# Kernel optimization log

Hardware: AMD Instinct MI355X
Metric: run time of the kernel (lower is better)

Reference implementation:

```python
import jax, jax.numpy as jnp
import numpy as np

NUM_HEADS = 8
EMBED_DIM = 512
EXPAND = 3
RPE_DIM = 512
RPE_LAYERS = 3
B, N = 4, 2048
D1 = (EXPAND * EMBED_DIM) // NUM_HEADS * NUM_HEADS  # 1536
HEAD_DIM = D1 // NUM_HEADS  # 192


def srms(x):
    # SimpleRMSNorm: x / (||x||_2 * d^{-1/2} + eps)
    d = x.shape[-1]
    rms = jnp.linalg.norm(x, axis=-1, keepdims=True) * (d ** -0.5)
    return x / (rms + 1e-8)


def rpe_net(idx, Wp, bp, Wl, bl, Wr, br):
    # idx: (m, 1) relative positions -> (m, h*head_dim)
    h = idx @ Wp.T + bp
    for i in range(Wl.shape[0]):  # fixed small layer count
        h = jax.nn.relu(srms(h)) @ Wl[i].T + bl[i]
    return jax.nn.relu(srms(h)) @ Wr.T + br


def setup_inputs() -> dict:
    key = jax.random.key(0)
    ks = jax.random.split(key, 12)
    s = 0.02
    return {
        "x": jax.random.normal(ks[0], (B, N, EMBED_DIM), jnp.float32),
        "Wu": jax.random.normal(ks[1], (D1, EMBED_DIM), jnp.float32) * s,
        "bu": jnp.zeros((D1,), jnp.float32),
        "Wv": jax.random.normal(ks[2], (D1, EMBED_DIM), jnp.float32) * s,
        "bv": jnp.zeros((D1,), jnp.float32),
        "Wo": jax.random.normal(ks[3], (EMBED_DIM, D1), jnp.float32) * s,
        "bo": jnp.zeros((EMBED_DIM,), jnp.float32),
        "Wp": jax.random.normal(ks[4], (RPE_DIM, 1), jnp.float32) * s,
        "bp": jax.random.normal(ks[5], (RPE_DIM,), jnp.float32) * s,
        "Wl": jax.random.normal(ks[6], (RPE_LAYERS, RPE_DIM, RPE_DIM), jnp.float32) * s,
        "bl": jax.random.normal(ks[7], (RPE_LAYERS, RPE_DIM), jnp.float32) * s,
        "Wr": jax.random.normal(ks[8], (NUM_HEADS * HEAD_DIM, RPE_DIM), jnp.float32) * s,
        "br": jax.random.normal(ks[9], (NUM_HEADS * HEAD_DIM,), jnp.float32) * s,
    }


def reference(x, Wu, bu, Wv, bv, Wo, bo, Wp, bp, Wl, bl, Wr, br):
    b, n, e = x.shape
    d1 = Wu.shape[0]
    hd = d1 // NUM_HEADS
    u = jax.nn.silu(x @ Wu.T + bu)                       # (b, n, d1)
    v = jax.nn.silu(x @ Wv.T + bv)                       # (b, n, d1)
    v = v.reshape(b, n, NUM_HEADS, hd).transpose(0, 2, 1, 3)  # (b, h, n, d)
    # Tno non-causal, par_type=1: indices [0, 1..n-1, 0, -(n-1)..-1]
    pos = jnp.arange(1, n, dtype=x.dtype)
    zero = jnp.zeros((1,), x.dtype)
    idx = jnp.concatenate([zero, pos, zero, -pos[::-1]])[:, None]  # (2n, 1)
    a = rpe_net(idx, Wp, bp, Wl, bl, Wr, br)             # (2n, h*d)
    a = a.reshape(2 * n, NUM_HEADS, hd).transpose(1, 0, 2)  # (h, 2n, d)
    m = 2 * n
    # circular conv of length 2n along sequence, truncate to n
    y = jnp.fft.rfft(v, m, axis=2) * jnp.fft.rfft(a, m, axis=1)[None]
    out = jnp.fft.irfft(y, m, axis=2)[:, :, :n, :]       # (b, h, n, d)
    out = out.transpose(0, 2, 1, 3).reshape(b, n, d1)    # (b, n, d1)
    return (u * out) @ Wo.T + bo
```

## Files before the change

### kernel.cpp

```cpp
#include <hip/hip_runtime.h>

#define N_SEQ 2048
#define M_FFT 4096
#define D1    1536
#define NH    8
#define HD    192
#define ED    512

typedef __bf16 bf16;
typedef __bf16 bf16x4 __attribute__((ext_vector_type(4)));
typedef __bf16 bf16x8 __attribute__((ext_vector_type(8)));
typedef float  floatx4 __attribute__((ext_vector_type(4)));
typedef float  cx __attribute__((ext_vector_type(2)));

enum { MODE_PLAIN = 0, MODE_SILU_UV = 1, MODE_AT = 3, MODE_RPE = 4 };

__device__ __forceinline__ void gload16(const void* g, void* l) {
    __builtin_amdgcn_global_load_lds(
        (const __attribute__((address_space(1))) void*)g,
        (__attribute__((address_space(3))) void*)l, 16, 0, 0);
}

template<int MODE, typename OutT>
__global__ __launch_bounds__(256) void gemm_bf16(
    const bf16* __restrict__ A, const bf16* __restrict__ Bw,
    const float* __restrict__ bias, const float* __restrict__ bias2,
    OutT* __restrict__ C, OutT* __restrict__ C2,
    int M, int Nc, int K,
    const float* __restrict__ scale_in, float* __restrict__ sumsq_out)
{
    __shared__ __align__(16) bf16 As[128 * 32];
    __shared__ __align__(16) bf16 Bs[128 * 32];

    const int tid  = threadIdx.x;
    const int row0 = blockIdx.y * 128;
    const int col0 = blockIdx.x * 128;
    const int wid  = tid >> 6;
    const int lane = tid & 63;
    const int lm   = lane & 15;
    const int lk   = lane >> 4;
    const int wm   = wid >> 1;
    const int wn   = wid & 1;
    const int ldrow  = tid >> 2;
    const int ldcol8 = (tid & 3) * 8;

    floatx4 acc[4][4] = {};

    const bf16* Ag = A  + ((size_t)(row0 + ldrow)) * K + ldcol8;
    const bf16* Bg = Bw + ((size_t)(col0 + ldrow)) * K + ldcol8;
    bf16* AsW = As + (wid * 16) * 32;
    bf16* BsW = Bs + (wid * 16) * 32;

    for (int k0 = 0; k0 < K; k0 += 32) {
        gload16(Ag + k0, AsW);
        gload16(Ag + (size_t)64 * K + k0, AsW + 64 * 32);
        gload16(Bg + k0, BsW);
        gload16(Bg + (size_t)64 * K + k0, BsW + 64 * 32);
        __syncthreads();

        bf16x8 af[4], bfr[4];
        #pragma unroll
        for (int mi = 0; mi < 4; ++mi)
            af[mi] = *(const bf16x8*)&As[(wm * 64 + mi * 16 + lm) * 32 + lk * 8];
        #pragma unroll
        for (int nj = 0; nj < 4; ++nj)
            bfr[nj] = *(const bf16x8*)&Bs[(wn * 64 + nj * 16 + lm) * 32 + lk * 8];
        #pragma unroll
        for (int mi = 0; mi < 4; ++mi)
            #pragma unroll
            for (int nj = 0; nj < 4; ++nj)
                acc[mi][nj] = __builtin_amdgcn_mfma_f32_16x16x32_bf16(
                    af[mi], bfr[nj], acc[mi][nj], 0, 0, 0);
        __syncthreads();
    }

    const float* bs = bias;
    OutT* dst = C;
    int cadj = 0;
    if (MODE == MODE_SILU_UV && col0 >= D1) { bs = bias2; dst = C2; cadj = D1; }

    float bcol[4];
    #pragma unroll
    for (int nj = 0; nj < 4; ++nj)
        bcol[nj] = bs[col0 - cadj + wn * 64 + nj * 16 + lm];

    if (MODE == MODE_RPE) {
        #pragma unroll
        for (int mi = 0; mi < 4; ++mi) {
            #pragma unroll
            for (int r = 0; r < 4; ++r) {
                const int row = row0 + wm * 64 + mi * 16 + lk * 4 + r;
                float sc = 1.0f;
                if (scale_in)
                    sc = 1.0f / (sqrtf(scale_in[row]) * 0.04419417382415922f + 1e-8f);
                float ssq = 0.0f;
                #pragma unroll
                for (int nj = 0; nj < 4; ++nj) {
                    const int col = col0 + wn * 64 + nj * 16 + lm;
                    float val = acc[mi][nj][r] * sc + bcol[nj];
                    ssq += val * val;
                    ((bf16*)C)[(size_t)row * Nc + col] = (bf16)fmaxf(val, 0.0f);
                }
                ssq += __shfl_xor(ssq, 1, 64);
                ssq += __shfl_xor(ssq, 2, 64);
                ssq += __shfl_xor(ssq, 4, 64);
                ssq += __shfl_xor(ssq, 8, 64);
                if (lm == 0) atomicAdd(&sumsq_out[row], ssq);
            }
        }
        return;
    }

    #pragma unroll
    for (int mi = 0; mi < 4; ++mi) {
        const int rbase = row0 + wm * 64 + mi * 16 + lk * 4;
        float sc[4];
        #pragma unroll
        for (int r = 0; r < 4; ++r) {
            sc[r] = 1.0f;
            if (MODE == MODE_AT && scale_in)
                sc[r] = 1.0f / (sqrtf(scale_in[rbase + r]) * 0.04419417382415922f + 1e-8f);
        }
        #pragma unroll
        for (int nj = 0; nj < 4; ++nj) {
            const int col = col0 - cadj + wn * 64 + nj * 16 + lm;
            float vals[4];
            #pragma unroll
            for (int r = 0; r < 4; ++r) {
                float val = acc[mi][nj][r] * sc[r] + bcol[nj];
                if (MODE == MODE_SILU_UV)
                    val = val / (1.0f + __expf(-val));
                vals[r] = val;
            }
            if (MODE == MODE_SILU_UV) {
                int b = rbase >> 11, s = rbase & 2047;
                bf16x4 o;
                #pragma unroll
                for (int r = 0; r < 4; ++r) o[r] = (bf16)vals[r];
                *(bf16x4*)&((bf16*)dst)[((size_t)(b * D1 + col)) * N_SEQ + s] = o;
            } else if (MODE == MODE_AT) {
                float4 o = make_float4(vals[0], vals[1], vals[2], vals[3]);
                *(float4*)&((float*)C)[(size_t)col * M + rbase] = o;
            } else {
                #pragma unroll
                for (int r = 0; r < 4; ++r)
                    C[(size_t)(rbase + r) * Nc + col] = (OutT)vals[r];
            }
        }
    }
}

__global__ __launch_bounds__(256) void f2b_all_kernel(
    const float* __restrict__ x,  const float* __restrict__ s0,
    const float* __restrict__ s1, const float* __restrict__ s2,
    const float* __restrict__ s3, const float* __restrict__ s4,
    const float* __restrict__ Wp, const float* __restrict__ bp,
    bf16* __restrict__ x_bf, bf16* __restrict__ w_bf,
    float* __restrict__ sumsq, bf16* __restrict__ g0,
    float* __restrict__ twd)
{
    const int bid = blockIdx.x;
    const int tid = threadIdx.x;
    __shared__ float red[4];

    if (bid < 7936) {
        const float* src;
        bf16* dst;
        size_t off;
        if (bid < 4096) {
            src = x; dst = x_bf; off = (size_t)bid * 1024;
        } else {
            int t = bid - 4096;
            int seg = t / 768;
            src = seg == 0 ? s0 : seg == 1 ? s1 : seg == 2 ? s2
                : seg == 3 ? s3 : s4;
            dst = w_bf + (size_t)seg * 786432;
            off = (size_t)(t % 768) * 1024;
        }
        size_t i = off + (size_t)tid * 4;
        float4 f = *(const float4*)(src + i);
        union { bf16 h[4]; short4 s; } u4;
        u4.h[0] = (bf16)f.x; u4.h[1] = (bf16)f.y;
        u4.h[2] = (bf16)f.z; u4.h[3] = (bf16)f.w;
        *(short4*)(dst + i) = u4.s;
    } else if (bid < 7948) {
        size_t i = (size_t)(bid - 7936) * 1024 + (size_t)tid * 4;
        *(float4*)(sumsq + i) = make_float4(0.f, 0.f, 0.f, 0.f);
    } else if (bid < 12044) {
        const int j = bid - 7948;
        float idxv = (j < N_SEQ) ? (float)j
                                 : (j == N_SEQ ? 0.0f : (float)(j - 2 * N_SEQ));
        float h1 = idxv * Wp[tid] + bp[tid];
        float h2 = idxv * Wp[tid + 256] + bp[tid + 256];
        float ss = h1 * h1 + h2 * h2;
        #pragma unroll
        for (int off = 32; off > 0; off >>= 1) ss += __shfl_down(ss, off, 64);
        if ((tid & 63) == 0) red[tid >> 6] = ss;
        __syncthreads();
        float tot = red[0] + red[1] + red[2] + red[3];
        float scale = 1.0f / (sqrtf(tot) * 0.04419417382415922f + 1e-8f);
        g0[(size_t)j * ED + tid]       = (bf16)fmaxf(h1 * scale, 0.0f);
        g0[(size_t)j * ED + tid + 256] = (bf16)fmaxf(h2 * scale, 0.0f);
    } else {
        const int idx = (bid - 12044) * 256 + tid;
        const int j = idx >> 4, tau = idx & 15;
        float sA, cA;
        __sincosf(-6.283185307179586f * (float)(j * tau) * (1.0f / 4096.0f),
                  &sA, &cA);
        cx w; w.x = cA; w.y = sA;
        ((cx*)twd)[idx] = w;
    }
}

#define FFT_LDS_SZ 4381

__device__ __forceinline__ int fpad(int i) { return i + (i >> 4) + 2 * (i >> 8); }

__device__ __forceinline__ cx mkcx(float a, float b) { cx r; r.x = a; r.y = b; return r; }
__device__ __forceinline__ cx cmul(cx a, cx b) {
    cx br = mkcx(-b.y, b.x);
    return a.xx * b + a.yy * br;
}
__device__ __forceinline__ cx cmul_cj(cx a, cx b) {
    cx bc = mkcx(b.x, -b.y);
    cx br = mkcx(b.y, b.x);
    return a.xx * bc + a.yy * br;
}
__device__ __forceinline__ cx cneg_i(cx a) { return mkcx(a.y, -a.x); }
__device__ __forceinline__ cx cpos_i(cx a) { return mkcx(-a.y, a.x); }
__host__ __device__ constexpr int brev4(int t) {
    return ((t & 1) << 3) | ((t & 2) << 1) | ((t & 4) >> 1) | ((t & 8) >> 3);
}

#define CC1 0.9238795325112867f
#define SS1 0.3826834323650898f
#define RR2 0.7071067811865476f

template<bool HZ>
__device__ __forceinline__ void fft16_dif_r4(cx x[16]) {
    const cx W1 = mkcx( CC1, -SS1);
    const cx W2 = mkcx( RR2, -RR2);
    const cx W3 = mkcx( SS1, -CC1);
    const cx W6 = mkcx(-RR2, -RR2);
    const cx W9 = mkcx(-CC1,  SS1);
    #pragma unroll
    for (int n = 0; n < 4; ++n) {
        cx A, B, C, D;
        if (HZ) { A = x[n]; C = x[n]; B = x[n + 4]; D = x[n + 4]; }
        else {
            A = x[n] + x[n + 8];      C = x[n] - x[n + 8];
            B = x[n + 4] + x[n + 12]; D = x[n + 4] - x[n + 12];
        }
        cx s = A - B;
        cx nid = cneg_i(D);
        cx m = C + nid;
        cx p = C - nid;
        x[n] = A + B;
        if (n == 0)      { x[4] = s;            x[8]  = m;           x[12] = p; }
        else if (n == 1) { x[5] = cmul(s, W2);  x[9]  = cmul(m, W1); x[13] = cmul(p, W3); }
        else if (n == 2) { x[6] = cneg_i(s);    x[10] = cmul(m, W2); x[14] = cmul(p, W6); }
        else             { x[7] = cmul(s, W6);  x[11] = cmul(m, W3); x[15] = cmul(p, W9); }
    }
    #pragma unroll
    for (int q = 0; q < 16; q += 4) {
        cx a = x[q], b = x[q + 1], c = x[q + 2], d = x[q + 3];
        cx a1 = a + c, c1 = a - c;
        cx b1 = b + d, d1 = cneg_i(b - d);
        x[q]     = a1 + b1;
        x[q + 1] = a1 - b1;
        x[q + 2] = c1 + d1;
        x[q + 3] = c1 - d1;
    }
}

template<bool HALF_OUT>
__device__ __forceinline__ void fft16_dit_inv_r4(cx x[16]) {
    const cx V1 = mkcx( CC1, SS1);
    const cx V2 = mkcx( RR2, RR2);
    const cx V3 = mkcx( SS1, CC1);
    const cx V6 = mkcx(-RR2, RR2);
    #pragma unroll
    for (int q = 0; q < 16; q += 4) {
        cx a = x[q], b = x[q + 1], c = x[q + 2], d = x[q + 3];
        cx a1 = a + b, b1 = a - b;
        cx c1 = c + d, d1 = c - d;
        cx t = cpos_i(d1);
        x[q]     = a1 + c1;
        x[q + 2] = a1 - c1;
        x[q + 1] = b1 + t;
        x[q + 3] = b1 - t;
    }
    #pragma unroll
    for (int n = 0; n < 4; ++n) {
        cx t1, t2;
        if (n == 0)      { t1 = x[4];             t2 = x[12]; }
        else if (n == 1) { t1 = cmul(x[5],  V2);  t2 = cmul(x[13], V2); }
        else if (n == 2) { t1 = cpos_i(x[6]);     t2 = cpos_i(x[14]); }
        else             { t1 = cmul(x[7],  V6);  t2 = cmul(x[15], V6); }
        cx P = x[n] + t1, Q = x[n] - t1;
        cx R = x[n + 8] + t2, S = x[n + 8] - t2;
        cx t, u;
        if (n == 0)      { t = R;            u = S; }
        else if (n == 1) { t = cmul(R, V1);  u = cmul(S, V1); }
        else if (n == 2) { t = cmul(R, V2);  u = cmul(S, V2); }
        else             { t = cmul(R, V3);  u = cmul(S, V3); }
        cx iu = cpos_i(u);
        x[n]     = P + t;
        x[n + 4] = Q + iu;
        if (!HALF_OUT) {
            x[n + 8]  = P - t;
            x[n + 12] = Q - iu;
        }
    }
}

template<bool CONJ>
__device__ __forceinline__ void apply_tw(cx v[16], const cx tw[16]) {
    #pragma unroll
    for (int tau = 1; tau < 16; ++tau) {
        const int q = brev4(tau);
        v[q] = CONJ ? cmul_cj(v[q], tw[tau]) : cmul(v[q], tw[tau]);
    }
}

template<bool HALF_ZERO, bool PF>
__device__ __forceinline__ void fft4096_fwd(
    cx* d, int tid, const cx* __restrict__ Twd,
    const float4* A0p, const float4* A1p,
    float4 a0pf[8], float4 a1pf[8])
{
    cx v[16], tw[16], tw2[16];
    {
        const cx* Tr1 = Twd + (tid << 4);
        const cx* Tr2 = Twd + ((tid & 15) << 8);
        #pragma unroll
        for (int t = 1; t < 16; ++t) tw[t] = Tr1[t];
        #pragma unroll
        for (int t = 1; t < 16; ++t) tw2[t] = Tr2[t];
    }
    {
        cx* base = d + fpad(tid);
        if (HALF_ZERO) {
            #pragma unroll
            for (int t = 0; t < 8; ++t) v[t] = base[274 * t];
            fft16_dif_r4<true>(v);
        } else {
            #pragma unroll
            for (int t = 0; t < 16; ++t) v[t] = base[274 * t];
            fft16_dif_r4<false>(v);
        }
        apply_tw<false>(v, tw);
        #pragma unroll
        for (int p = 0; p < 16; ++p) base[274 * p] = v[p];
    }
    __syncthreads();
    {
        cx* base = d + fpad(((tid >> 4) << 8) + (tid & 15));
        #pragma unroll
        for (int t = 0; t < 16; ++t) v[t] = base[17 * t];
        fft16_dif_r4<false>(v);
        apply_tw<false>(v, tw2);
        #pragma unroll
        for (int p = 0; p < 16; ++p) base[17 * p] = v[p];
    }
    __syncthreads();
    if (PF) {
        #pragma unroll
        for (int i = 0; i < 8; ++i) { a0pf[i] = A0p[i]; a1pf[i] = A1p[i]; }
        __builtin_amdgcn_sched_barrier(0);
    }
    {
        cx* base = d + fpad(tid << 4);
        #pragma unroll
        for (int t = 0; t < 16; ++t) v[t] = base[t];
        fft16_dif_r4<false>(v);
        #pragma unroll
        for (int p = 0; p < 16; ++p) base[p] = v[p];
    }
    __syncthreads();
}

__global__ __launch_bounds__(256, 4) void fft_a_kernel(
    const float* a_t, cx* __restrict__ A0s, cx* A1s,
    const cx* __restrict__ Twd)
{
    __shared__ cx data[FFT_LDS_SZ];
    const int tid = threadIdx.x;
    const int r = blockIdx.x;

    const float* r0 = a_t + (size_t)(2 * r) * M_FFT;
    const float* r1 = r0 + M_FFT;
    {
        cx* base = data + fpad(tid);
        #pragma unroll
        for (int k = 0; k < 16; ++k)
            base[274 * k] = mkcx(r0[tid + 256 * k], r1[tid + 256 * k]);
    }
    __syncthreads();
    fft4096_fwd<false, false>(data, tid, Twd, nullptr, nullptr, nullptr, nullptr);

    const float c = 0.25f / 4096.0f;
    cx* A0row = A0s + (size_t)r * 4096;
    cx* A1row = A1s + (size_t)r * 4096;
    if (tid == 0) {
        #pragma unroll
        for (int i = 0; i < 16; ++i) {
            const int p2 = (i < 2) ? i : (i ^ ((1 << (31 - __clz(i))) - 1));
            cx Wk = data[fpad(i)];
            cx Wm = data[fpad(p2)];
            cx cjWm = mkcx(Wm.x, -Wm.y);
            A0row[i] = c * (Wk + cjWm);
            A1row[i] = c * cneg_i(Wk - cjWm);
        }
    } else {
        const int base = tid << 4;
        const int mask = (1 << (31 - __clz(base))) - 1;
        const cx* zb  = data + fpad(base);
        const cx* zb2 = data + fpad((base ^ mask) - 15);
        #pragma unroll
        for (int i = 0; i < 16; ++i) {
            cx Wk = zb[i];
            cx Wm = zb2[15 - i];
            cx cjWm = mkcx(Wm.x, -Wm.y);
            A0row[base + i] = c * (Wk + cjWm);
            A1row[base + i] = c * cneg_i(Wk - cjWm);
        }
    }
}

__global__ __launch_bounds__(256, 4) void fft_conv_kernel(
    const bf16* __restrict__ v_t, const cx* __restrict__ A0s,
    const cx* __restrict__ A1s, const bf16* __restrict__ u_t,
    bf16* __restrict__ gated_t, const cx* __restrict__ Twd)
{
    __shared__ cx data[FFT_LDS_SZ];
    const int tid = threadIdx.x;
    const int bx = blockIdx.x;
    const int xcd  = bx & 7;
    const int slot = bx >> 3;
    const int b    = slot & 3;
    const int r    = (slot >> 2) * 8 + xcd;
    const int ch = 2 * r;

    const bf16* z0 = v_t + ((size_t)(b * D1 + ch)) * N_SEQ;
    const bf16* z1 = z0 + N_SEQ;

    {
        const int s = tid * 8;
        cx* base = data + fpad(s);
        bf16x8 a0 = *(const bf16x8*)(z0 + s);
        bf16x8 a1 = *(const bf16x8*)(z1 + s);
        #pragma unroll
        for (int i = 0; i < 8; ++i)
            base[i] = mkcx((float)a0[i], (float)a1[i]);
    }
    __syncthreads();

    const int pbase = tid << 4;
    const cx* A0row = A0s + (size_t)r * 4096;
    const cx* A1row = A1s + (size_t)r * 4096;
    float4 a0pf[8], a1pf[8];
    fft4096_fwd<true, true>(data, tid, Twd,
                            (const float4*)(A0row + pbase),
                            (const float4*)(A1row + pbase), a0pf, a1pf);

    cx v[16], tw[16];
    {
        auto pf = [](const float4* p, int i) -> cx {
            return (i & 1) ? mkcx(p[i >> 1].z, p[i >> 1].w)
                           : mkcx(p[i >> 1].x, p[i >> 1].y);
        };
        if (tid == 0) {
            #pragma unroll
            for (int i = 0; i < 16; ++i) {
                const int p2 = (i < 2) ? i : (i ^ ((1 << (31 - __clz(i))) - 1));
                cx Zk = data[fpad(i)];
                cx Zm = data[fpad(p2)];
                cx cjZm = mkcx(Zm.x, -Zm.y);
                cx V0 = Zk + cjZm;
                cx V1 = cneg_i(Zk - cjZm);
                v[i] = cmul(V0, pf(a0pf, i)) + cpos_i(cmul(V1, pf(a1pf, i)));
            }
        } else {
            const int mask = (1 << (31 - __clz(pbase))) - 1;
            const cx* zb  = data + fpad(pbase);
            const cx* zb2 = data + fpad((pbase ^ mask) - 15);
            #pragma unroll
            for (int i = 0; i < 16; ++i) {
                cx Zk = zb[i];
                cx Zm = zb2[15 - i];
                cx cjZm = mkcx(Zm.x, -Zm.y);
                cx V0 = Zk + cjZm;
                cx V1 = cneg_i(Zk - cjZm);
                v[i] = cmul(V0, pf(a0pf, i)) + cpos_i(cmul(V1, pf(a1pf, i)));
            }
        }
        __syncthreads();
        fft16_dit_inv_r4<false>(v);
        cx* base = data + fpad(pbase);
        #pragma unroll
        for (int i = 0; i < 16; ++i) base[i] = v[i];
    }
    __syncthreads();

    const bf16* u0 = u_t + ((size_t)(b * D1 + ch)) * N_SEQ;
    const bf16* u1 = u0 + N_SEQ;
    bf16x8 ua = *(const bf16x8*)(u0 + tid * 8);
    bf16x8 ub = *(const bf16x8*)(u1 + tid * 8);
    __builtin_amdgcn_sched_barrier(0);

    {
        cx* base = data + fpad(((tid >> 4) << 8) + (tid & 15));
        const cx* Tr = Twd + ((tid & 15) << 8);
        #pragma unroll
        for (int t = 1; t < 16; ++t) tw[t] = Tr[t];
        #pragma unroll
        for (int p = 0; p < 16; ++p) v[p] = base[17 * p];
        apply_tw<true>(v, tw);
        fft16_dit_inv_r4<false>(v);
        #pragma unroll
        for (int t = 0; t < 16; ++t) base[17 * t] = v[t];
    }
    __syncthreads();
    {
        cx* base = data + fpad(tid);
        const cx* Tr = Twd + (tid << 4);
        #pragma unroll
        for (int t = 1; t < 16; ++t) tw[t] = Tr[t];
        #pragma unroll
        for (int p = 0; p < 16; ++p) v[p] = base[274 * p];
        apply_tw<true>(v, tw);
        fft16_dit_inv_r4<true>(v);
        #pragma unroll
        for (int t = 0; t < 8; ++t) base[274 * t] = v[t];
    }
    __syncthreads();

    bf16* g0 = gated_t + ((size_t)(b * D1 + ch)) * N_SEQ;
    bf16* g1 = g0 + N_SEQ;
    {
        const int t = tid * 8;
        const cx* base = data + fpad(t);
        bf16x8 oa, ob;
        #pragma unroll
        for (int i = 0; i < 8; ++i) {
            cx y = base[i];
            oa[i] = (bf16)(y.x * (float)ua[i]);
            ob[i] = (bf16)(y.y * (float)ub[i]);
        }
        *(bf16x8*)(g0 + t) = oa;
        *(bf16x8*)(g1 + t) = ob;
    }
}

__global__ __launch_bounds__(256) void transpose_cs_kernel(
    const bf16* __restrict__ in, bf16* __restrict__ outp)
{
    __shared__ bf16 tile[64 * 68];
    const int c0 = blockIdx.x * 64;
    const int m0 = blockIdx.y * 64;
    const int b  = m0 >> 11;
    const int s0 = m0 & 2047;
    const int tid = threadIdx.x;
    const int cl = tid >> 4;
    const int sc = (tid & 15) * 4;
    #pragma unroll
    for (int p = 0; p < 4; ++p) {
        int c = p * 16 + cl;
        bf16x4 v = *(const bf16x4*)&in[((size_t)(b * D1 + c0 + c)) * N_SEQ + s0 + sc];
        *(bf16x4*)&tile[c * 68 + sc] = v;
    }
    __syncthreads();
    const int sl = tid >> 4;
    const int cc = (tid & 15) * 4;
    #pragma unroll
    for (int p = 0; p < 4; ++p) {
        int s = p * 16 + sl;
        bf16x4 o;
        #pragma unroll
        for (int j = 0; j < 4; ++j) o[j] = tile[(cc + j) * 68 + s];
        *(bf16x4*)&outp[((size_t)(m0 + s)) * D1 + c0 + cc] = o;
    }
}

extern "C" void kernel_launch(void* const* d_in, const int* in_sizes, int n_in,
                              void* d_out, int out_size, void* d_ws, size_t ws_size,
                              hipStream_t stream)
{
    const float* x  = (const float*)d_in[0];
    const float* Wu = (const float*)d_in[1];
    const float* bu = (const float*)d_in[2];
    const float* Wv = (const float*)d_in[3];
    const float* bv = (const float*)d_in[4];
    const float* Wo = (const float*)d_in[5];
    const float* bo = (const float*)d_in[6];
    const float* Wp = (const float*)d_in[7];
    const float* bp = (const float*)d_in[8];
    const float* Wl = (const float*)d_in[9];
    const float* bl = (const float*)d_in[10];
    const float* Wr = (const float*)d_in[11];
    const float* br = (const float*)d_in[12];
    float* out = (float*)d_out;

    float* ws      = (float*)d_ws;
    float* a_t     = ws;
    float* A0spec  = a_t   + 6291456;
    float* sumsq   = A0spec + 6291456;
    float* twd     = sumsq + 12288;
    bf16*  bfws    = (bf16*)(twd + 8192);
    bf16*  x_bf    = bfws;
    bf16*  w_bf    = x_bf    + 4194304;
    bf16*  Wuv_bf  = w_bf;
    bf16*  Wo_bf   = w_bf    + 2 * 786432;
    bf16*  Wl_bf   = Wo_bf   + 786432;
    bf16*  Wr_bf   = Wl_bf   + 786432;
    bf16*  gA      = Wr_bf   + 786432;
    bf16*  gB      = gA      + 2097152;
    bf16*  u_t     = gB      + 2097152;
    bf16*  v_t     = u_t     + 12582912;
    bf16*  gated_t = v_t     + 12582912;
    bf16*  gated   = gated_t + 12582912;

    dim3 blk(256);

    f2b_all_kernel<<<4096 + 5 * 768 + 12 + 4096 + 16, blk, 0, stream>>>(
        x, Wu, Wv, Wo, Wl, Wr, Wp, bp, x_bf, w_bf, sumsq, gA, twd);

    gemm_bf16<MODE_SILU_UV, bf16><<<dim3(24, 64), blk, 0, stream>>>(
        x_bf, Wuv_bf, bu, bv, u_t, v_t, 8192, 2 * D1, ED, nullptr, nullptr);

    bf16* gin = gA;
    bf16* gout = gB;
    for (int i = 0; i < 3; ++i) {
        const float* sin_p = (i == 0) ? nullptr : sumsq + (size_t)(i - 1) * 4096;
        gemm_bf16<MODE_RPE, bf16><<<dim3(4, 32), blk, 0, stream>>>(
            gin, Wl_bf + (size_t)i * ED * ED, bl + (size_t)i * ED, nullptr,
            gout, nullptr, 4096, ED, ED, sin_p, sumsq + (size_t)i * 4096);
        bf16* t = gin; gin = gout; gout = t;
    }
    gemm_bf16<MODE_AT, float><<<dim3(12, 32), blk, 0, stream>>>(
        gin, Wr_bf, br, nullptr, a_t, nullptr, 4096, D1, ED,
        sumsq + 2 * 4096, nullptr);

    fft_a_kernel<<<768, blk, 0, stream>>>(
        a_t, (cx*)A0spec, (cx*)a_t, (const cx*)twd);
    fft_conv_kernel<<<3072, blk, 0, stream>>>(
        v_t, (const cx*)A0spec, (const cx*)a_t, u_t, gated_t, (const cx*)twd);

    transpose_cs_kernel<<<dim3(24, 128), blk, 0, stream>>>(gated_t, gated);

    gemm_bf16<MODE_PLAIN, float><<<dim3(4, 64), blk, 0, stream>>>(
        gated, Wo_bf, bo, nullptr, out, nullptr, 8192, ED, D1,
        nullptr, nullptr);
}
```

Before: 392.2 us.

## Load FFT inputs directly to registers and stage second twiddles in LDS

The FFT kernels now load the sequence inputs straight into registers in the stride-256 layout the first radix-16 pass needs. This removes the initial LDS write/read round trip and one barrier. The second-stage twiddles, shared by every thread with the same tid&15, are staged once into a small LDS table instead of each thread loading 15 values from global. First-stage twiddles stay in registers across forward and inverse passes, so they are no longer reloaded. The A-spectrum prefetch and the u gate loads move later, which reduces register pressure but removes their overlap with the FFT passes. Input loads become strided scalar bf16 reads rather than 16-byte vector reads, which may cost coalescing efficiency.

```diff
diff --git a/kernel.cpp b/kernel.cpp
--- a/kernel.cpp
+++ b/kernel.cpp
@@ -323,33 +323,24 @@
     }
 }
 
-template<bool HALF_ZERO, bool PF>
-__device__ __forceinline__ void fft4096_fwd(
-    cx* d, int tid, const cx* __restrict__ Twd,
-    const float4* A0p, const float4* A1p,
-    float4 a0pf[8], float4 a1pf[8])
+template<bool CONJ>
+__device__ __forceinline__ void apply_tw_lds(cx v[16], const cx* twrow) {
+    #pragma unroll
+    for (int tau = 1; tau < 16; ++tau) {
+        cx w = twrow[tau * 16];
+        const int q = brev4(tau);
+        v[q] = CONJ ? cmul_cj(v[q], w) : cmul(v[q], w);
+    }
+}
+
+template<bool HALF_ZERO>
+__device__ __forceinline__ void fft4096_fwd_core(
+    cx* d, int tid, const cx tw[16], const cx* tw2lds, cx v[16])
 {
-    cx v[16], tw[16], tw2[16];
-    {
-        const cx* Tr1 = Twd + (tid << 4);
-        const cx* Tr2 = Twd + ((tid & 15) << 8);
-        #pragma unroll
-        for (int t = 1; t < 16; ++t) tw[t] = Tr1[t];
-        #pragma unroll
-        for (int t = 1; t < 16; ++t) tw2[t] = Tr2[t];
-    }
-    {
+    {
+        fft16_dif_r4<HALF_ZERO>(v);
+        apply_tw<false>(v, tw);
         cx* base = d + fpad(tid);
-        if (HALF_ZERO) {
-            #pragma unroll
-            for (int t = 0; t < 8; ++t) v[t] = base[274 * t];
-            fft16_dif_r4<true>(v);
-        } else {
-            #pragma unroll
-            for (int t = 0; t < 16; ++t) v[t] = base[274 * t];
-            fft16_dif_r4<false>(v);
-        }
-        apply_tw<false>(v, tw);
         #pragma unroll
         for (int p = 0; p < 16; ++p) base[274 * p] = v[p];
     }
@@ -359,16 +350,11 @@
         #pragma unroll
         for (int t = 0; t < 16; ++t) v[t] = base[17 * t];
         fft16_dif_r4<false>(v);
-        apply_tw<false>(v, tw2);
+        apply_tw_lds<false>(v, tw2lds + (tid & 15));
         #pragma unroll
         for (int p = 0; p < 16; ++p) base[17 * p] = v[p];
     }
     __syncthreads();
-    if (PF) {
-        #pragma unroll
-        for (int i = 0; i < 8; ++i) { a0pf[i] = A0p[i]; a1pf[i] = A1p[i]; }
-        __builtin_amdgcn_sched_barrier(0);
-    }
     {
         cx* base = d + fpad(tid << 4);
         #pragma unroll
@@ -385,19 +371,26 @@
     const cx* __restrict__ Twd)
 {
     __shared__ cx data[FFT_LDS_SZ];
+    __shared__ cx tw2lds[256];
     const int tid = threadIdx.x;
     const int r = blockIdx.x;
 
+    cx tw[16];
+    {
+        const cx* Tr1 = Twd + (tid << 4);
+        #pragma unroll
+        for (int t = 1; t < 16; ++t) tw[t] = Tr1[t];
+        tw2lds[(tid >> 4) * 16 + (tid & 15)] = Twd[(tid & 15) * 256 + (tid >> 4)];
+    }
+
     const float* r0 = a_t + (size_t)(2 * r) * M_FFT;
     const float* r1 = r0 + M_FFT;
-    {
-        cx* base = data + fpad(tid);
-        #pragma unroll
-        for (int k = 0; k < 16; ++k)
-            base[274 * k] = mkcx(r0[tid + 256 * k], r1[tid + 256 * k]);
-    }
-    __syncthreads();
-    fft4096_fwd<false, false>(data, tid, Twd, nullptr, nullptr, nullptr, nullptr);
+    cx v[16];
+    #pragma unroll
+    for (int t = 0; t < 16; ++t)
+        v[t] = mkcx(r0[tid + 256 * t], r1[tid + 256 * t]);
+
+    fft4096_fwd_core<false>(data, tid, tw, tw2lds, v);
 
     const float c = 0.25f / 4096.0f;
     cx* A0row = A0s + (size_t)r * 4096;
@@ -434,6 +427,7 @@
     bf16* __restrict__ gated_t, const cx* __restrict__ Twd)
 {
     __shared__ cx data[FFT_LDS_SZ];
+    __shared__ cx tw2lds[256];
     const int tid = threadIdx.x;
     const int bx = blockIdx.x;
     const int xcd  = bx & 7;
@@ -442,30 +436,34 @@
     const int r    = (slot >> 2) * 8 + xcd;
     const int ch = 2 * r;
 
+    cx tw[16];
+    {
+        const cx* Tr1 = Twd + (tid << 4);
+        #pragma unroll
+        for (int t = 1; t < 16; ++t) tw[t] = Tr1[t];
+        tw2lds[(tid >> 4) * 16 + (tid & 15)] = Twd[(tid & 15) * 256 + (tid >> 4)];
+    }
+
     const bf16* z0 = v_t + ((size_t)(b * D1 + ch)) * N_SEQ;
     const bf16* z1 = z0 + N_SEQ;
-
-    {
-        const int s = tid * 8;
-        cx* base = data + fpad(s);
-        bf16x8 a0 = *(const bf16x8*)(z0 + s);
-        bf16x8 a1 = *(const bf16x8*)(z1 + s);
-        #pragma unroll
-        for (int i = 0; i < 8; ++i)
-            base[i] = mkcx((float)a0[i], (float)a1[i]);
-    }
-    __syncthreads();
-
-    const int pbase = tid << 4;
+    cx v[16];
+    #pragma unroll
+    for (int t = 0; t < 8; ++t)
+        v[t] = mkcx((float)z0[tid + 256 * t], (float)z1[tid + 256 * t]);
+
+    fft4096_fwd_core<true>(data, tid, tw, tw2lds, v);
+
     const cx* A0row = A0s + (size_t)r * 4096;
     const cx* A1row = A1s + (size_t)r * 4096;
-    float4 a0pf[8], a1pf[8];
-    fft4096_fwd<true, true>(data, tid, Twd,
-                            (const float4*)(A0row + pbase),
-                            (const float4*)(A1row + pbase), a0pf, a1pf);
-
-    cx v[16], tw[16];
-    {
+    const int pbase = tid << 4;
+    {
+        float4 a0pf[8], a1pf[8];
+        {
+            const float4* A0p = (const float4*)(A0row + pbase);
+            const float4* A1p = (const float4*)(A1row + pbase);
+            #pragma unroll
+            for (int i = 0; i < 8; ++i) { a0pf[i] = A0p[i]; a1pf[i] = A1p[i]; }
+        }
         auto pf = [](const float4* p, int i) -> cx {
             return (i & 1) ? mkcx(p[i >> 1].z, p[i >> 1].w)
                            : mkcx(p[i >> 1].x, p[i >> 1].y);
@@ -502,21 +500,11 @@
         for (int i = 0; i < 16; ++i) base[i] = v[i];
     }
     __syncthreads();
-
-    const bf16* u0 = u_t + ((size_t)(b * D1 + ch)) * N_SEQ;
-    const bf16* u1 = u0 + N_SEQ;
-    bf16x8 ua = *(const bf16x8*)(u0 + tid * 8);
-    bf16x8 ub = *(const bf16x8*)(u1 + tid * 8);
-    __builtin_amdgcn_sched_barrier(0);
-
     {
         cx* base = data + fpad(((tid >> 4) << 8) + (tid & 15));
-        const cx* Tr = Twd + ((tid & 15) << 8);
-        #pragma unroll
-        for (int t = 1; t < 16; ++t) tw[t] = Tr[t];
         #pragma unroll
         for (int p = 0; p < 16; ++p) v[p] = base[17 * p];
-        apply_tw<true>(v, tw);
+        apply_tw_lds<true>(v, tw2lds + (tid & 15));
         fft16_dit_inv_r4<false>(v);
         #pragma unroll
         for (int t = 0; t < 16; ++t) base[17 * t] = v[t];
@@ -524,9 +512,6 @@
     __syncthreads();
     {
         cx* base = data + fpad(tid);
-        const cx* Tr = Twd + (tid << 4);
-        #pragma unroll
-        for (int t = 1; t < 16; ++t) tw[t] = Tr[t];
         #pragma unroll
         for (int p = 0; p < 16; ++p) v[p] = base[274 * p];
         apply_tw<true>(v, tw);
@@ -536,11 +521,15 @@
     }
     __syncthreads();
 
+    const bf16* u0 = u_t + ((size_t)(b * D1 + ch)) * N_SEQ;
+    const bf16* u1 = u0 + N_SEQ;
     bf16* g0 = gated_t + ((size_t)(b * D1 + ch)) * N_SEQ;
     bf16* g1 = g0 + N_SEQ;
     {
         const int t = tid * 8;
         const cx* base = data + fpad(t);
+        bf16x8 ua = *(const bf16x8*)(u0 + t);
+        bf16x8 ub = *(const bf16x8*)(u1 + t);
         bf16x8 oa, ob;
         #pragma unroll
         for (int i = 0; i < 8; ++i) {
```

After: 370.2 us. 1.06x faster.
